# Performance work log

Measured on AMD Instinct MI355X. Metric: run time of the kernel, lower is better.

The kernel has to match this reference:

```python
import jax, jax.numpy as jnp
import numpy as np

GROUPS = 8
NEG_SLOPE = 0.1
EPS = 1e-5


def group_norm(x, gamma, beta):
    # x: (B, N, C). Matches torch GroupNorm applied on (B, C, N):
    # normalize over (channels-in-group, N) per batch per group.
    B, N, C = x.shape
    xg = x.reshape(B, N, GROUPS, C // GROUPS)
    mean = xg.mean(axis=(1, 3), keepdims=True)
    var = xg.var(axis=(1, 3), keepdims=True)
    xg = (xg - mean) * jax.lax.rsqrt(var + EPS)
    return xg.reshape(B, N, C) * gamma + beta


def unary_block(x, W, b, gamma, beta):
    # Linear -> GroupNorm -> LeakyReLU(0.1)
    h = jnp.einsum('bnc,cd->bnd', x, W) + b
    h = group_norm(h, gamma, beta)
    return jnp.where(h >= 0, h, NEG_SLOPE * h)


def setup_inputs() -> dict:
    key = jax.random.key(0)
    ks = jax.random.split(key, 16)
    B, N, M, K, Cin, Cout = 4, 8192, 32768, 16, 128, 128
    inp = {
        'q_feats': jax.random.normal(ks[0], (B, N, Cin), jnp.float32),
        's_feats': jax.random.normal(ks[1], (B, M, Cin), jnp.float32),
        'q_points': jax.random.normal(ks[2], (B, N, 3), jnp.float32),
        's_points': jax.random.normal(ks[3], (B, N, K, 3), jnp.float32),
        'downsample_indices': jax.random.randint(ks[4], (B, N, K), 0, M, jnp.int32),
    }
    sc1 = 1.0 / np.sqrt(Cin)
    sc2 = 1.0 / np.sqrt(Cout)
    inp['W1'] = jax.random.uniform(ks[5], (Cin, Cout), jnp.float32, -sc1, sc1)
    inp['b1'] = jnp.zeros((Cout,), jnp.float32)
    inp['g1'] = jnp.ones((Cout,), jnp.float32)
    inp['be1'] = jnp.zeros((Cout,), jnp.float32)
    inp['W2'] = jax.random.uniform(ks[6], (Cout, Cout), jnp.float32, -sc2, sc2)
    inp['b2'] = jnp.zeros((Cout,), jnp.float32)
    inp['g2'] = jnp.ones((Cout,), jnp.float32)
    inp['be2'] = jnp.zeros((Cout,), jnp.float32)
    inp['W3'] = jax.random.uniform(ks[7], (Cout, Cout), jnp.float32, -sc2, sc2)
    inp['b3'] = jnp.zeros((Cout,), jnp.float32)
    inp['g3'] = jnp.ones((Cout,), jnp.float32)
    inp['be3'] = jnp.zeros((Cout,), jnp.float32)
    return inp


def reference(q_feats, s_feats, q_points, s_points, downsample_indices,
              W1, b1, g1, be1, W2, b2, g2, be2, W3, b3, g3, be3):
    # knn_gather: (B, N, K, C) gathered from (B, M, C)
    grouped = jax.vmap(lambda f, i: f[i])(s_feats, downsample_indices)
    # inverse-squared-distance weights over K neighbors
    d2 = jnp.sum((s_points - q_points[:, :, None, :]) ** 2, axis=-1)  # (B,N,K)
    w = 1.0 / (d2 + 1e-8)
    w = w / jnp.sum(w, axis=-1, keepdims=True)
    latent = jnp.sum(grouped * w[..., None], axis=2)  # (B,N,C)
    h = unary_block(latent, W1, b1, g1, be1)
    h = unary_block(h, W2, b2, g2, be2)
    return unary_block(h + q_feats, W3, b3, g3, be3)
```

## Files before the change

### kernel.cpp

```cpp
#include <hip/hip_runtime.h>


constexpr int NPB = 8192;
constexpr int BN  = 32768;
constexpr int CH  = 128;
constexpr int KNB = 16;
constexpr int MS  = 32768;
constexpr int NG  = 8;
constexpr int CG  = 16;
constexpr int RPB = 64;
constexpr int NBLK = BN / RPB;
constexpr int BPB  = NPB / RPB;
constexpr int MRPB = 16;
constexpr int MNBLK = BN / MRPB;
constexpr int MBPB  = NPB / MRPB;
constexpr int XS = 152;

typedef short short8 __attribute__((ext_vector_type(8)));
typedef float floatx4 __attribute__((ext_vector_type(4)));

static __device__ __forceinline__ unsigned short f2bs(float f) {
    unsigned int u = __builtin_bit_cast(unsigned int, f);
    unsigned int r = (u + 0x7fffu + ((u >> 16) & 1u)) >> 16;
    return (unsigned short)r;
}
static __device__ __forceinline__ float bs2f(unsigned short s) {
    unsigned int u = ((unsigned int)s) << 16;
    return __builtin_bit_cast(float, u);
}

__global__ __launch_bounds__(256) void k_prep(
    const float* __restrict__ W1, const float* __restrict__ W2,
    const float* __restrict__ W3,
    unsigned short* __restrict__ Wf1, unsigned short* __restrict__ Wf2,
    unsigned short* __restrict__ Wf3)
{
    const int bi = blockIdx.x;
    const int w  = bi >> 6;
    const int i  = bi & 63;
    const int el = i * 256 + threadIdx.x;
    const int n  = el >> 7, k = el & 127;
    const float* W = (w == 0) ? W1 : (w == 1) ? W2 : W3;
    unsigned short v = f2bs(W[k * 128 + n]);
    unsigned short* Wf = (w == 0) ? Wf1 : (w == 1) ? Wf2 : Wf3;
    int j = n >> 4, lr = n & 15;
    int kt = k >> 5, qd = (k >> 3) & 3, e = k & 7;
    Wf[(((j * 4 + kt) * 64) + (qd * 16 + lr)) * 8 + e] = v;
}

__global__ __launch_bounds__(256) void k_head(
    const float* __restrict__ sf, const float* __restrict__ qp,
    const float* __restrict__ sp, const int* __restrict__ idx,
    const unsigned short* __restrict__ Wf,
    const float* __restrict__ bias,
    unsigned short* __restrict__ hout,
    float* __restrict__ part_out)
{
    const int rep = blockIdx.x & 7;
    const int q8  = blockIdx.x >> 3;
    const int bi  = (rep >> 1) * BPB + (rep & 1) * 64 + q8;
    const int b   = rep >> 1;
    const int t   = threadIdx.x;

    __shared__ unsigned short Xl[RPB * XS];
    __shared__ float wv[RPB * KNB];
    __shared__ float winv[RPB];
    __shared__ float pw[4][16];

    #pragma unroll
    for (int i = 0; i < 4; i++) {
        int p = i * 256 + t;
        int row = p >> 4, k = p & 15;
        size_t rg = (size_t)bi * RPB + row;
        float qx = qp[rg * 3 + 0], qy = qp[rg * 3 + 1], qz = qp[rg * 3 + 2];
        const float* spp = sp + (rg * KNB + k) * 3;
        float dx = spp[0] - qx, dy = spp[1] - qy, dz = spp[2] - qz;
        wv[p] = 1.0f / (dx * dx + dy * dy + dz * dz + 1e-8f);
    }
    __syncthreads();
    if (t < RPB) {
        float s = 0.f;
        #pragma unroll
        for (int k = 0; k < KNB; k++) s += wv[t * KNB + k];
        winv[t] = 1.0f / s;
    }
    __syncthreads();
    {
        const int grp = t >> 5, c4 = (t & 31) * 4;
        for (int rr = 0; rr < 8; rr++) {
            int row = grp * 8 + rr;
            size_t rg = (size_t)bi * RPB + row;
            const int* ip = idx + rg * KNB;
            float ax = 0.f, ay = 0.f, az = 0.f, aw = 0.f;
            #pragma unroll
            for (int k = 0; k < KNB; k++) {
                int j = ip[k];
                const float4 f = *(const float4*)(sf + ((size_t)b * MS + j) * CH + c4);
                float w = wv[row * KNB + k];
                ax += w * f.x; ay += w * f.y; az += w * f.z; aw += w * f.w;
            }
            float wi = winv[row];
            ushort4 pk;
            pk.x = f2bs(ax * wi); pk.y = f2bs(ay * wi);
            pk.z = f2bs(az * wi); pk.w = f2bs(aw * wi);
            *(ushort4*)&Xl[row * XS + c4] = pk;
        }
    }
    __syncthreads();

    const int w  = t >> 6;
    const int l  = t & 63;
    const int lr = l & 15;
    const int qd = l >> 4;
    floatx4 acc[8] = {};
    #pragma unroll
    for (int kt = 0; kt < 4; kt++) {
        short8 a = *(const short8*)&Xl[(w * 16 + lr) * XS + kt * 32 + qd * 8];
        #pragma unroll
        for (int j = 0; j < 8; j++) {
            short8 bf = *(const short8*)(Wf + (((j * 4 + kt) * 64) + l) * 8);
            acc[j] = __builtin_amdgcn_mfma_f32_16x16x32_bf16(a, bf, acc[j], 0, 0, 0);
        }
    }

    float vals[8][4];
    #pragma unroll
    for (int j = 0; j < 8; j++) {
        float bj = bias[j * 16 + lr];
        float ss = 0.f, qq = 0.f;
        #pragma unroll
        for (int r = 0; r < 4; r++) {
            float v = acc[j][r] + bj;
            vals[j][r] = v;
            ss += v; qq += v * v;
        }
        #pragma unroll
        for (int off = 32; off; off >>= 1) {
            ss += __shfl_down(ss, off);
            qq += __shfl_down(qq, off);
        }
        if (l == 0) { pw[w][j] = ss; pw[w][8 + j] = qq; }
    }
    #pragma unroll
    for (int j = 0; j < 8; j++)
        #pragma unroll
        for (int r = 0; r < 4; r++)
            Xl[(w * 16 + qd * 4 + r) * XS + j * 16 + lr] = f2bs(vals[j][r]);
    __syncthreads();
    if (t < 16)
        part_out[(size_t)bi * 16 + t] = pw[0][t] + pw[1][t] + pw[2][t] + pw[3][t];
    #pragma unroll
    for (int i = 0; i < 4; i++) {
        int flat = i * 2048 + t * 8;
        int row = flat >> 7, col = flat & 127;
        *(short8*)(hout + (size_t)bi * RPB * CH + flat) =
            *(const short8*)&Xl[row * XS + col];
    }
}

template <int RESID, int PPB>
__global__ __launch_bounds__(256) void k_mid(
    const unsigned short* __restrict__ hin,
    const float* __restrict__ part_in,
    const float* __restrict__ gamma,
    const float* __restrict__ beta,
    const float* __restrict__ qf,
    const unsigned short* __restrict__ Wf,
    const float* __restrict__ bias,
    unsigned short* __restrict__ hout,
    float* __restrict__ part_out)
{
    const int bi = blockIdx.x;
    const int t  = threadIdx.x;
    const int b  = bi / MBPB;

    __shared__ unsigned short Xl[MRPB * XS];
    __shared__ float red[16][17];
    __shared__ float2 stats_s[NG];
    __shared__ float pw[4][4];

    constexpr int R = PPB / 16;
    {
        int j = t & 15, chunk = t >> 4;
        float acc = 0.f;
        #pragma unroll
        for (int i = 0; i < R; i++)
            acc += part_in[(size_t)(b * PPB + chunk * R + i) * 16 + j];
        red[chunk][j] = acc;
    }
    __syncthreads();
    if (t < NG) {
        float s = 0.f, q = 0.f;
        #pragma unroll
        for (int c = 0; c < 16; c++) { s += red[c][t]; q += red[c][t + 8]; }
        const float cnt = (float)(NPB * CG);
        float mean = s / cnt;
        float var  = q / cnt - mean * mean;
        stats_s[t] = make_float2(mean, rsqrtf(var + 1e-5f));
    }
    __syncthreads();

    {
        int flat = t * 8;
        int row = flat >> 7, col = flat & 127;
        size_t gidx = (size_t)bi * (MRPB * CH) + flat;
        short8 hv = *(const short8*)(hin + gidx);
        float2 st = stats_s[col >> 4];
        float4 g0 = *(const float4*)(gamma + col);
        float4 g1 = *(const float4*)(gamma + col + 4);
        float4 b0 = *(const float4*)(beta + col);
        float4 b1 = *(const float4*)(beta + col + 4);
        float gg[8] = {g0.x, g0.y, g0.z, g0.w, g1.x, g1.y, g1.z, g1.w};
        float bb[8] = {b0.x, b0.y, b0.z, b0.w, b1.x, b1.y, b1.z, b1.w};
        float re[8];
        if (RESID) {
            float4 r0 = *(const float4*)(qf + gidx);
            float4 r1 = *(const float4*)(qf + gidx + 4);
            re[0]=r0.x; re[1]=r0.y; re[2]=r0.z; re[3]=r0.w;
            re[4]=r1.x; re[5]=r1.y; re[6]=r1.z; re[7]=r1.w;
        }
        unsigned short ov[8];
        #pragma unroll
        for (int e = 0; e < 8; e++) {
            float v = bs2f((unsigned short)hv[e]);
            float y = (v - st.x) * st.y * gg[e] + bb[e];
            y = (y >= 0.f) ? y : 0.1f * y;
            if (RESID) y += re[e];
            ov[e] = f2bs(y);
        }
        *(short8*)&Xl[row * XS + col] = *(short8*)ov;
    }
    __syncthreads();

    const int w  = t >> 6;
    const int l  = t & 63;
    const int lr = l & 15;
    const int qd = l >> 4;
    floatx4 acc2[2] = {};
    #pragma unroll
    for (int kt = 0; kt < 4; kt++) {
        short8 a = *(const short8*)&Xl[lr * XS + kt * 32 + qd * 8];
        #pragma unroll
        for (int jj = 0; jj < 2; jj++) {
            int j = w * 2 + jj;
            short8 bf = *(const short8*)(Wf + (((j * 4 + kt) * 64) + l) * 8);
            acc2[jj] = __builtin_amdgcn_mfma_f32_16x16x32_bf16(a, bf, acc2[jj], 0, 0, 0);
        }
    }

    float vals[2][4];
    #pragma unroll
    for (int jj = 0; jj < 2; jj++) {
        int j = w * 2 + jj;
        float bj = bias[j * 16 + lr];
        float ss = 0.f, qq = 0.f;
        #pragma unroll
        for (int r = 0; r < 4; r++) {
            float v = acc2[jj][r] + bj;
            vals[jj][r] = v;
            ss += v; qq += v * v;
        }
        #pragma unroll
        for (int off = 32; off; off >>= 1) {
            ss += __shfl_down(ss, off);
            qq += __shfl_down(qq, off);
        }
        if (l == 0) { pw[w][jj] = ss; pw[w][2 + jj] = qq; }
    }
    __syncthreads();

    #pragma unroll
    for (int jj = 0; jj < 2; jj++)
        #pragma unroll
        for (int r = 0; r < 4; r++)
            Xl[(qd * 4 + r) * XS + (w * 2 + jj) * 16 + lr] = f2bs(vals[jj][r]);
    if (t < 8)
        part_out[(size_t)bi * 16 + t] = pw[t >> 1][t & 1];
    else if (t < 16) {
        int g = t - 8;
        part_out[(size_t)bi * 16 + t] = pw[g >> 1][2 + (g & 1)];
    }
    __syncthreads();

    {
        int flat = t * 8;
        int row = flat >> 7, col = flat & 127;
        *(short8*)(hout + (size_t)bi * (MRPB * CH) + flat) =
            *(const short8*)&Xl[row * XS + col];
    }
}

__global__ __launch_bounds__(256) void k_out(
    const unsigned short* __restrict__ hin, const float* __restrict__ part_in,
    const float* __restrict__ gamma, const float* __restrict__ beta,
    float* __restrict__ out)
{
    const int bi = blockIdx.x;
    const int t  = threadIdx.x;
    const int b  = bi / MBPB;
    __shared__ float red[16][17];
    __shared__ float2 stats_s[NG];
    constexpr int PPB = 512;
    constexpr int R = PPB / 16;
    {
        int j = t & 15, chunk = t >> 4;
        float acc = 0.f;
        #pragma unroll
        for (int i = 0; i < R; i++)
            acc += part_in[(size_t)(b * PPB + chunk * R + i) * 16 + j];
        red[chunk][j] = acc;
    }
    __syncthreads();
    if (t < NG) {
        float s = 0.f, q = 0.f;
        #pragma unroll
        for (int c = 0; c < 16; c++) { s += red[c][t]; q += red[c][t + 8]; }
        const float cnt = (float)(NPB * CG);
        float mean = s / cnt;
        float var  = q / cnt - mean * mean;
        stats_s[t] = make_float2(mean, rsqrtf(var + 1e-5f));
    }
    __syncthreads();
    {
        int flat = t * 8;
        int col = flat & 127;
        size_t gidx = (size_t)bi * (MRPB * CH) + flat;
        short8 hv = *(const short8*)(hin + gidx);
        float2 st = stats_s[col >> 4];
        float4 g0 = *(const float4*)(gamma + col);
        float4 g1 = *(const float4*)(gamma + col + 4);
        float4 b0 = *(const float4*)(beta + col);
        float4 b1 = *(const float4*)(beta + col + 4);
        float gg[8] = {g0.x, g0.y, g0.z, g0.w, g1.x, g1.y, g1.z, g1.w};
        float bb[8] = {b0.x, b0.y, b0.z, b0.w, b1.x, b1.y, b1.z, b1.w};
        float o[8];
        #pragma unroll
        for (int e = 0; e < 8; e++) {
            float v = bs2f((unsigned short)hv[e]);
            float y = (v - st.x) * st.y * gg[e] + bb[e];
            o[e] = (y >= 0.f) ? y : 0.1f * y;
        }
        float4 o0 = {o[0], o[1], o[2], o[3]};
        float4 o1 = {o[4], o[5], o[6], o[7]};
        *(float4*)(out + gidx)     = o0;
        *(float4*)(out + gidx + 4) = o1;
    }
}

extern "C" void kernel_launch(void* const* d_in, const int* in_sizes, int n_in,
                              void* d_out, int out_size, void* d_ws, size_t ws_size,
                              hipStream_t stream) {
    const float* qf  = (const float*)d_in[0];
    const float* sf  = (const float*)d_in[1];
    const float* qp  = (const float*)d_in[2];
    const float* sp  = (const float*)d_in[3];
    const int*   idx = (const int*)  d_in[4];
    const float* W1  = (const float*)d_in[5];
    const float* b1  = (const float*)d_in[6];
    const float* g1  = (const float*)d_in[7];
    const float* be1 = (const float*)d_in[8];
    const float* W2  = (const float*)d_in[9];
    const float* b2  = (const float*)d_in[10];
    const float* g2  = (const float*)d_in[11];
    const float* be2 = (const float*)d_in[12];
    const float* W3  = (const float*)d_in[13];
    const float* b3  = (const float*)d_in[14];
    const float* g3  = (const float*)d_in[15];
    const float* be3 = (const float*)d_in[16];

    char* ws = (char*)d_ws;
    unsigned short* Wf1 = (unsigned short*)(ws);
    unsigned short* Wf2 = (unsigned short*)(ws + 32768);
    unsigned short* Wf3 = (unsigned short*)(ws + 65536);
    float* p1 = (float*)(ws + 98304);
    float* p2 = (float*)(ws + 131072);
    float* p3 = (float*)(ws + 262144);
    unsigned short* h1 = (unsigned short*)(ws + 393216);
    unsigned short* h2 = (unsigned short*)(ws + 393216 + 8388608);
    unsigned short* h3 = (unsigned short*)(ws + 393216 + 2 * 8388608);
    float* out = (float*)d_out;

    k_prep<<<192, 256, 0, stream>>>(W1, W2, W3, Wf1, Wf2, Wf3);
    k_head<<<NBLK, 256, 0, stream>>>(sf, qp, sp, idx, Wf1, b1, h1, p1);
    k_mid<0, 128><<<MNBLK, 256, 0, stream>>>(h1, p1, g1, be1, nullptr, Wf2, b2, h2, p2);
    k_mid<1, 512><<<MNBLK, 256, 0, stream>>>(h2, p2, g2, be2, qf, Wf3, b3, h3, p3);
    k_out<<<MNBLK, 256, 0, stream>>>(h3, p3, g3, be3, out);
}
```

Before: 193.0 us.

## Shrink head kernel blocks to 16 rows to quadruple grid parallelism

The gather+first-linear head kernel now processes 16 rows per block instead of 64, launching four times as many blocks. Each wave computes two output column tiles of a single 16-row MFMA tile instead of eight tiles for its own rows. Partial GroupNorm statistics now come per 16-row block, so the workspace offsets and the downstream reduction counts are updated to match. This is meant to raise occupancy and latency hiding for the irregular neighbour gather, at the cost of more blocks, more partial-sum entries and reloading weights per block.

```diff
diff --git a/kernel.cpp b/kernel.cpp
--- a/kernel.cpp
+++ b/kernel.cpp
@@ -8,9 +8,6 @@
 constexpr int MS  = 32768;
 constexpr int NG  = 8;
 constexpr int CG  = 16;
-constexpr int RPB = 64;
-constexpr int NBLK = BN / RPB;
-constexpr int BPB  = NPB / RPB;
 constexpr int MRPB = 16;
 constexpr int MNBLK = BN / MRPB;
 constexpr int MBPB  = NPB / MRPB;
@@ -58,27 +55,25 @@
 {
     const int rep = blockIdx.x & 7;
     const int q8  = blockIdx.x >> 3;
-    const int bi  = (rep >> 1) * BPB + (rep & 1) * 64 + q8;
+    const int bi  = (rep >> 1) * MBPB + (rep & 1) * 256 + q8;
     const int b   = rep >> 1;
     const int t   = threadIdx.x;
 
-    __shared__ unsigned short Xl[RPB * XS];
-    __shared__ float wv[RPB * KNB];
-    __shared__ float winv[RPB];
-    __shared__ float pw[4][16];
-
-    #pragma unroll
-    for (int i = 0; i < 4; i++) {
-        int p = i * 256 + t;
-        int row = p >> 4, k = p & 15;
-        size_t rg = (size_t)bi * RPB + row;
+    __shared__ unsigned short Xl[MRPB * XS];
+    __shared__ float wv[MRPB * KNB];
+    __shared__ float winv[MRPB];
+    __shared__ float pw[4][4];
+
+    {
+        int row = t >> 4, k = t & 15;
+        size_t rg = (size_t)bi * MRPB + row;
         float qx = qp[rg * 3 + 0], qy = qp[rg * 3 + 1], qz = qp[rg * 3 + 2];
         const float* spp = sp + (rg * KNB + k) * 3;
         float dx = spp[0] - qx, dy = spp[1] - qy, dz = spp[2] - qz;
-        wv[p] = 1.0f / (dx * dx + dy * dy + dz * dz + 1e-8f);
-    }
-    __syncthreads();
-    if (t < RPB) {
+        wv[t] = 1.0f / (dx * dx + dy * dy + dz * dz + 1e-8f);
+    }
+    __syncthreads();
+    if (t < MRPB) {
         float s = 0.f;
         #pragma unroll
         for (int k = 0; k < KNB; k++) s += wv[t * KNB + k];
@@ -87,9 +82,9 @@
     __syncthreads();
     {
         const int grp = t >> 5, c4 = (t & 31) * 4;
-        for (int rr = 0; rr < 8; rr++) {
-            int row = grp * 8 + rr;
-            size_t rg = (size_t)bi * RPB + row;
+        for (int rr = 0; rr < 2; rr++) {
+            int row = grp * 2 + rr;
+            size_t rg = (size_t)bi * MRPB + row;
             const int* ip = idx + rg * KNB;
             float ax = 0.f, ay = 0.f, az = 0.f, aw = 0.f;
             #pragma unroll
@@ -112,26 +107,28 @@
     const int l  = t & 63;
     const int lr = l & 15;
     const int qd = l >> 4;
-    floatx4 acc[8] = {};
+    floatx4 acc2[2] = {};
     #pragma unroll
     for (int kt = 0; kt < 4; kt++) {
-        short8 a = *(const short8*)&Xl[(w * 16 + lr) * XS + kt * 32 + qd * 8];
-        #pragma unroll
-        for (int j = 0; j < 8; j++) {
+        short8 a = *(const short8*)&Xl[lr * XS + kt * 32 + qd * 8];
+        #pragma unroll
+        for (int jj = 0; jj < 2; jj++) {
+            int j = w * 2 + jj;
             short8 bf = *(const short8*)(Wf + (((j * 4 + kt) * 64) + l) * 8);
-            acc[j] = __builtin_amdgcn_mfma_f32_16x16x32_bf16(a, bf, acc[j], 0, 0, 0);
-        }
-    }
-
-    float vals[8][4];
-    #pragma unroll
-    for (int j = 0; j < 8; j++) {
+            acc2[jj] = __builtin_amdgcn_mfma_f32_16x16x32_bf16(a, bf, acc2[jj], 0, 0, 0);
+        }
+    }
+
+    float vals[2][4];
+    #pragma unroll
+    for (int jj = 0; jj < 2; jj++) {
+        int j = w * 2 + jj;
         float bj = bias[j * 16 + lr];
         float ss = 0.f, qq = 0.f;
         #pragma unroll
         for (int r = 0; r < 4; r++) {
-            float v = acc[j][r] + bj;
-            vals[j][r] = v;
+            float v = acc2[jj][r] + bj;
+            vals[jj][r] = v;
             ss += v; qq += v * v;
         }
         #pragma unroll
@@ -139,26 +136,32 @@
             ss += __shfl_down(ss, off);
             qq += __shfl_down(qq, off);
         }
-        if (l == 0) { pw[w][j] = ss; pw[w][8 + j] = qq; }
-    }
-    #pragma unroll
-    for (int j = 0; j < 8; j++)
+        if (l == 0) { pw[w][jj] = ss; pw[w][2 + jj] = qq; }
+    }
+    __syncthreads();
+
+    #pragma unroll
+    for (int jj = 0; jj < 2; jj++)
         #pragma unroll
         for (int r = 0; r < 4; r++)
-            Xl[(w * 16 + qd * 4 + r) * XS + j * 16 + lr] = f2bs(vals[j][r]);
-    __syncthreads();
-    if (t < 16)
-        part_out[(size_t)bi * 16 + t] = pw[0][t] + pw[1][t] + pw[2][t] + pw[3][t];
-    #pragma unroll
-    for (int i = 0; i < 4; i++) {
-        int flat = i * 2048 + t * 8;
+            Xl[(qd * 4 + r) * XS + (w * 2 + jj) * 16 + lr] = f2bs(vals[jj][r]);
+    if (t < 8)
+        part_out[(size_t)bi * 16 + t] = pw[t >> 1][t & 1];
+    else if (t < 16) {
+        int g = t - 8;
+        part_out[(size_t)bi * 16 + t] = pw[g >> 1][2 + (g & 1)];
+    }
+    __syncthreads();
+
+    {
+        int flat = t * 8;
         int row = flat >> 7, col = flat & 127;
-        *(short8*)(hout + (size_t)bi * RPB * CH + flat) =
+        *(short8*)(hout + (size_t)bi * (MRPB * CH) + flat) =
             *(const short8*)&Xl[row * XS + col];
     }
 }
 
-template <int RESID, int PPB>
+template <int RESID>
 __global__ __launch_bounds__(256) void k_mid(
     const unsigned short* __restrict__ hin,
     const float* __restrict__ part_in,
@@ -179,13 +182,13 @@
     __shared__ float2 stats_s[NG];
     __shared__ float pw[4][4];
 
-    constexpr int R = PPB / 16;
+    constexpr int R = 32;
     {
         int j = t & 15, chunk = t >> 4;
         float acc = 0.f;
         #pragma unroll
         for (int i = 0; i < R; i++)
-            acc += part_in[(size_t)(b * PPB + chunk * R + i) * 16 + j];
+            acc += part_in[(size_t)(b * 512 + chunk * R + i) * 16 + j];
         red[chunk][j] = acc;
     }
     __syncthreads();
@@ -300,14 +303,13 @@
     const int b  = bi / MBPB;
     __shared__ float red[16][17];
     __shared__ float2 stats_s[NG];
-    constexpr int PPB = 512;
-    constexpr int R = PPB / 16;
+    constexpr int R = 32;
     {
         int j = t & 15, chunk = t >> 4;
         float acc = 0.f;
         #pragma unroll
         for (int i = 0; i < R; i++)
-            acc += part_in[(size_t)(b * PPB + chunk * R + i) * 16 + j];
+            acc += part_in[(size_t)(b * 512 + chunk * R + i) * 16 + j];
         red[chunk][j] = acc;
     }
     __syncthreads();
@@ -373,16 +375,16 @@
     unsigned short* Wf2 = (unsigned short*)(ws + 32768);
     unsigned short* Wf3 = (unsigned short*)(ws + 65536);
     float* p1 = (float*)(ws + 98304);
-    float* p2 = (float*)(ws + 131072);
-    float* p3 = (float*)(ws + 262144);
-    unsigned short* h1 = (unsigned short*)(ws + 393216);
-    unsigned short* h2 = (unsigned short*)(ws + 393216 + 8388608);
-    unsigned short* h3 = (unsigned short*)(ws + 393216 + 2 * 8388608);
+    float* p2 = (float*)(ws + 229376);
+    float* p3 = (float*)(ws + 360448);
+    unsigned short* h1 = (unsigned short*)(ws + 524288);
+    unsigned short* h2 = (unsigned short*)(ws + 524288 + 8388608);
+    unsigned short* h3 = (unsigned short*)(ws + 524288 + 2 * 8388608);
     float* out = (float*)d_out;
 
     k_prep<<<192, 256, 0, stream>>>(W1, W2, W3, Wf1, Wf2, Wf3);
-    k_head<<<NBLK, 256, 0, stream>>>(sf, qp, sp, idx, Wf1, b1, h1, p1);
-    k_mid<0, 128><<<MNBLK, 256, 0, stream>>>(h1, p1, g1, be1, nullptr, Wf2, b2, h2, p2);
-    k_mid<1, 512><<<MNBLK, 256, 0, stream>>>(h2, p2, g2, be2, qf, Wf3, b3, h3, p3);
+    k_head<<<MNBLK, 256, 0, stream>>>(sf, qp, sp, idx, Wf1, b1, h1, p1);
+    k_mid<0><<<MNBLK, 256, 0, stream>>>(h1, p1, g1, be1, nullptr, Wf2, b2, h2, p2);
+    k_mid<1><<<MNBLK, 256, 0, stream>>>(h2, p2, g2, be2, qf, Wf3, b3, h3, p3);
     k_out<<<MNBLK, 256, 0, stream>>>(h3, p3, g3, be3, out);
 }
```

New measurement: 190.9 us. About the same (-1.1%).
